# Optimization experiments

Measured on AMD Instinct MI355X. Metric: run time of the kernel, lower is better.

## Reference

```python
import jax, jax.numpy as jnp
import numpy as np

LEAKY_SLOPE = 0.01  # torch nn.LeakyReLU default


def leaky_relu(x):
    return jnp.where(x >= 0, x, LEAKY_SLOPE * x)


def rgcn_conv(x, edge_index, edge_type, w_rel, w_root, b_conv):
    # PyG RGCNConv: out = x @ W_root + b + sum_r mean_{edges of rel r into i}(x_src @ W_r)
    n = x.shape[0]
    src, dst = edge_index[0], edge_index[1]
    out = x @ w_root + b_conv
    num_rel = w_rel.shape[0]
    for r in range(num_rel):  # small fixed relation count
        mask = (edge_type == r)
        msg = x[src] @ w_rel[r]                      # [E, H]
        msg = jnp.where(mask[:, None], msg, 0.0)
        agg = jax.ops.segment_sum(msg, dst, num_segments=n)          # [N, H]
        cnt = jax.ops.segment_sum(mask.astype(x.dtype), dst, num_segments=n)
        out = out + agg / jnp.maximum(cnt, 1.0)[:, None]             # mean aggr
    return out


def setup_inputs() -> dict:
    key = jax.random.key(0)
    ks = jax.random.split(key, 10)
    N, E, D_IN, H, OUT, R = 50000, 600000, 768, 128, 3, 2
    s_in = 1.0 / np.sqrt(D_IN)
    s_h = 1.0 / np.sqrt(H)
    return {
        "feature": jax.random.normal(ks[0], (N, D_IN), dtype=jnp.float32),
        "edge_index": jax.random.randint(ks[1], (2, E), 0, N, dtype=jnp.int64),
        "edge_type": jax.random.randint(ks[2], (E,), 0, R, dtype=jnp.int64),
        "w_in": jax.random.uniform(ks[3], (D_IN, H), jnp.float32, -s_in, s_in),
        "b_in": jax.random.uniform(ks[4], (H,), jnp.float32, -s_in, s_in),
        "w_rel": jax.random.uniform(ks[5], (R, H, H), jnp.float32, -s_h, s_h),
        "w_root": jax.random.uniform(ks[6], (H, H), jnp.float32, -s_h, s_h),
        "b_conv": jnp.zeros((H,), jnp.float32),
        "w_out": jax.random.uniform(ks[7], (H, OUT), jnp.float32, -s_h, s_h),
        "b_out": jax.random.uniform(ks[8], (OUT,), jnp.float32, -s_h, s_h),
    }


def reference(feature, edge_index, edge_type, w_in, b_in, w_rel, w_root, b_conv, w_out, b_out):
    x = leaky_relu(feature @ w_in + b_in)
    # NOTE: original forward applies rgcn1 twice (shared weights); dropout is
    # identity at inference; rgcn2/linear_relu_output1 are unused.
    x = rgcn_conv(x, edge_index, edge_type, w_rel, w_root, b_conv)
    x = rgcn_conv(x, edge_index, edge_type, w_rel, w_root, b_conv)
    return x @ w_out + b_out
```

## Files before the change

kernel.cpp:

```cpp
#include <hip/hip_runtime.h>

#define H 128
#define CAP 64

typedef _Float16 f16x8 __attribute__((ext_vector_type(8)));
typedef float    f32x4 __attribute__((ext_vector_type(4)));

__global__ __launch_bounds__(256) void hist_fill(const int* __restrict__ src,
    const int* __restrict__ dst, const int* __restrict__ et,
    int* __restrict__ cnt, int* __restrict__ elist, int E, int N)
{
    int e = blockIdx.x * 256 + threadIdx.x;
    if (e >= E) return;
    int s = src[e], d = dst[e], t = et[e];
    int b = t * N + d;
    int pos = atomicAdd(&cnt[b], 1);
    if (pos < CAP) elist[(size_t)b * CAP + pos] = s;
}

__global__ __launch_bounds__(256) void prep_w(const float* __restrict__ w_in,
    const float* __restrict__ w_root, const float* __restrict__ w_rel,
    _Float16* __restrict__ wInT, _Float16* __restrict__ w3T, int K)
{
    int idx = blockIdx.x * 256 + threadIdx.x;
    int tot1 = K * H;
    if (idx < tot1) {
        int k = idx >> 7, c = idx & 127;
        int o = ((k >> 3) << 10) + (c << 3) + (k & 7);
        wInT[o] = (_Float16)w_in[idx];
    } else {
        int i2 = idx - tot1;
        if (i2 < 3 * H * H) {
            int m = i2 / (H * H), r2 = i2 - m * (H * H);
            int c = r2 >> 7, k = r2 & 127;
            const float* s = (m == 0) ? w_root : (w_rel + (size_t)(m - 1) * H * H);
            w3T[i2] = (_Float16)s[(size_t)k * H + c];
        }
    }
}

__device__ __forceinline__ f16x8 cvt8(float4 v0, float4 v1) {
    f16x8 t;
    t[0] = (_Float16)v0.x; t[1] = (_Float16)v0.y; t[2] = (_Float16)v0.z; t[3] = (_Float16)v0.w;
    t[4] = (_Float16)v1.x; t[5] = (_Float16)v1.y; t[6] = (_Float16)v1.z; t[7] = (_Float16)v1.w;
    return t;
}

__global__ __launch_bounds__(256, 3) void gemm_big(const float* __restrict__ A,
    const _Float16* __restrict__ WP, const float* __restrict__ bias,
    _Float16* __restrict__ C16, int M, int K)
{
    const int tid = threadIdx.x;
    const int w   = tid >> 6;
    const int l   = tid & 63;
    const int l15 = l & 15;
    const int q   = l >> 4;
    const int wrow = blockIdx.x * 64 + w * 16;

    int r0 = wrow + l15; if (r0 >= M) r0 = M - 1;
    const float* ap = A + (size_t)r0 * K + q * 8;
    const _Float16* bp = WP + ((size_t)q * H + l15) * 8;

    float bj[8];
#pragma unroll
    for (int j = 0; j < 8; j++) bj[j] = bias[j * 16 + l15];

    f32x4 acc[8];
    const f32x4 z4 = {0.f, 0.f, 0.f, 0.f};
#pragma unroll
    for (int j = 0; j < 8; j++) acc[j] = z4;

    float4 aA0, aA1; f16x8 bA[8];
    float4 aB0, aB1; f16x8 bB[8];

    aA0 = *(const float4*)(ap);
    aA1 = *(const float4*)(ap + 4);
#pragma unroll
    for (int j = 0; j < 8; j++) bA[j] = *(const f16x8*)(bp + j * 128);

    const int steps = K / 32;
    for (int s = 0; s < steps; s += 2) {
        {
            const int k1 = (s + 1) * 32;
            aB0 = *(const float4*)(ap + k1);
            aB1 = *(const float4*)(ap + k1 + 4);
            const _Float16* nb = bp + (size_t)(s + 1) * 4096;
#pragma unroll
            for (int j = 0; j < 8; j++) bB[j] = *(const f16x8*)(nb + j * 128);
        }
        {
            f16x8 af = cvt8(aA0, aA1);
#pragma unroll
            for (int j = 0; j < 8; j++)
                acc[j] = __builtin_amdgcn_mfma_f32_16x16x32_f16(af, bA[j], acc[j], 0, 0, 0);
        }
        if (s + 2 < steps) {
            const int k2 = (s + 2) * 32;
            aA0 = *(const float4*)(ap + k2);
            aA1 = *(const float4*)(ap + k2 + 4);
            const _Float16* nb = bp + (size_t)(s + 2) * 4096;
#pragma unroll
            for (int j = 0; j < 8; j++) bA[j] = *(const f16x8*)(nb + j * 128);
        }
        {
            f16x8 af = cvt8(aB0, aB1);
#pragma unroll
            for (int j = 0; j < 8; j++)
                acc[j] = __builtin_amdgcn_mfma_f32_16x16x32_f16(af, bB[j], acc[j], 0, 0, 0);
        }
    }

#pragma unroll
    for (int rg = 0; rg < 4; rg++) {
        int row = wrow + q * 4 + rg;
        if (row < M) {
#pragma unroll
            for (int j = 0; j < 8; j++) {
                float v = acc[j][rg] + bj[j];
                v = (v >= 0.f) ? v : 0.01f * v;
                C16[(size_t)row * H + j * 16 + l15] = (_Float16)v;
            }
        }
    }
}

__global__ __launch_bounds__(512) void gemm3(const _Float16* __restrict__ X16,
    const _Float16* __restrict__ W3, const float* __restrict__ bias,
    float* __restrict__ Y, _Float16* __restrict__ Hh, int M, int mtiles,
    size_t NH)
{
    const int w   = threadIdx.x >> 6;
    const int l   = threadIdx.x & 63;
    const int l15 = l & 15;
    const int q   = l >> 4;
    const int col = w * 16 + l15;

    f16x8 bf[3][4];
#pragma unroll
    for (int m = 0; m < 3; m++) {
        const _Float16* wpp = W3 + (size_t)m * H * H + (size_t)col * H + q * 8;
#pragma unroll
        for (int c = 0; c < 4; c++) bf[m][c] = *(const f16x8*)(wpp + c * 32);
    }
    const float bj = bias[col];

    int t = blockIdx.x;
    if (t >= mtiles) return;
    f16x8 xf[4];
    {
        const _Float16* xp = X16 + ((size_t)t * 16 + l15) * H + q * 8;
#pragma unroll
        for (int c = 0; c < 4; c++) xf[c] = *(const f16x8*)(xp + c * 32);
    }

    const f32x4 z4 = {0.f, 0.f, 0.f, 0.f};
    while (true) {
        int tn = t + gridDim.x;
        bool more = tn < mtiles;
        f16x8 xnf[4];
        if (more) {
            const _Float16* xp = X16 + ((size_t)tn * 16 + l15) * H + q * 8;
#pragma unroll
            for (int c = 0; c < 4; c++) xnf[c] = *(const f16x8*)(xp + c * 32);
        }

        f32x4 a0 = z4, a1 = z4, a2 = z4;
#pragma unroll
        for (int c = 0; c < 4; c++) {
            a0 = __builtin_amdgcn_mfma_f32_16x16x32_f16(xf[c], bf[0][c], a0, 0, 0, 0);
            a1 = __builtin_amdgcn_mfma_f32_16x16x32_f16(xf[c], bf[1][c], a1, 0, 0, 0);
            a2 = __builtin_amdgcn_mfma_f32_16x16x32_f16(xf[c], bf[2][c], a2, 0, 0, 0);
        }

#pragma unroll
        for (int rg = 0; rg < 4; rg++) {
            int row = t * 16 + q * 4 + rg;
            if (row < M) {
                Y [(size_t)row * H + col]      = a0[rg] + bj;
                Hh[(size_t)row * H + col]      = (_Float16)a1[rg];
                Hh[NH + (size_t)row * H + col] = (_Float16)a2[rg];
            }
        }
        if (!more) break;
        t = tn;
#pragma unroll
        for (int c = 0; c < 4; c++) xf[c] = xnf[c];
    }
}

template<int DO_OUT>
__global__ __launch_bounds__(256) void gather_mean(const float* __restrict__ Y,
    const _Float16* __restrict__ h, const int* __restrict__ elist,
    const int* __restrict__ cnt, _Float16* __restrict__ xn, int N, size_t NH,
    const float* __restrict__ Wo, const float* __restrict__ bo,
    float* __restrict__ out)
{
    int wv = blockIdx.x * 4 + (threadIdx.x >> 6);
    int l  = threadIdx.x & 63;
    if (wv >= N) return;

    int d0r = cnt[wv], d1r = cnt[N + wv];
    int d0 = d0r < CAP ? d0r : CAP;
    int d1 = d1r < CAP ? d1r : CAP;
    float inv0 = d0r > 0 ? 1.f / (float)d0r : 0.f;
    float inv1 = d1r > 0 ? 1.f / (float)d1r : 0.f;
    const int* l0 = elist + (size_t)wv * CAP;
    const int* l1 = elist + ((size_t)N + wv) * CAP;
    const int tot = d0 + d1;

    const int eo = l >> 4;
    const int c8 = (l & 15) * 8;

    float wo0[8], wo1[8], wo2[8];
    if (DO_OUT) {
#pragma unroll
        for (int j = 0; j < 8; j++) {
            wo0[j] = Wo[(c8 + j) * 3 + 0];
            wo1[j] = Wo[(c8 + j) * 3 + 1];
            wo2[j] = Wo[(c8 + j) * 3 + 2];
        }
    }

    float acc[8];
#pragma unroll
    for (int j = 0; j < 8; j++) acc[j] = 0.f;

    const f16x8 zv = {};
    for (int p = eo; p < tot; p += 16) {
        int p1 = p + 4, p2 = p + 8, p3 = p + 12;
        bool fA = p < d0;
        int   sA  = fA ? l0[p] : l1[p - d0];
        float scA = fA ? inv0 : inv1;
        f16x8 vA  = *(const f16x8*)&h[(fA ? (size_t)0 : NH) + (size_t)sA * H + c8];
        f16x8 vB = zv, vC = zv, vD = zv;
        float scB = 0.f, scC = 0.f, scD = 0.f;
        if (p1 < tot) {
            bool f = p1 < d0;
            int s = f ? l0[p1] : l1[p1 - d0];
            scB = f ? inv0 : inv1;
            vB = *(const f16x8*)&h[(f ? (size_t)0 : NH) + (size_t)s * H + c8];
        }
        if (p2 < tot) {
            bool f = p2 < d0;
            int s = f ? l0[p2] : l1[p2 - d0];
            scC = f ? inv0 : inv1;
            vC = *(const f16x8*)&h[(f ? (size_t)0 : NH) + (size_t)s * H + c8];
        }
        if (p3 < tot) {
            bool f = p3 < d0;
            int s = f ? l0[p3] : l1[p3 - d0];
            scD = f ? inv0 : inv1;
            vD = *(const f16x8*)&h[(f ? (size_t)0 : NH) + (size_t)s * H + c8];
        }
#pragma unroll
        for (int j = 0; j < 8; j++)
            acc[j] += scA * (float)vA[j] + scB * (float)vB[j]
                    + scC * (float)vC[j] + scD * (float)vD[j];
    }

#pragma unroll
    for (int j = 0; j < 8; j++) {
        acc[j] += __shfl_xor(acc[j], 16);
        acc[j] += __shfl_xor(acc[j], 32);
    }

    float4 y0 = *(const float4*)&Y[(size_t)wv * H + c8];
    float4 y1 = *(const float4*)&Y[(size_t)wv * H + c8 + 4];
    float xv[8];
    xv[0] = acc[0] + y0.x; xv[1] = acc[1] + y0.y;
    xv[2] = acc[2] + y0.z; xv[3] = acc[3] + y0.w;
    xv[4] = acc[4] + y1.x; xv[5] = acc[5] + y1.y;
    xv[6] = acc[6] + y1.z; xv[7] = acc[7] + y1.w;

    if (DO_OUT) {
        float p0 = 0.f, p1 = 0.f, p2 = 0.f;
#pragma unroll
        for (int j = 0; j < 8; j++) {
            p0 += xv[j] * wo0[j];
            p1 += xv[j] * wo1[j];
            p2 += xv[j] * wo2[j];
        }
#pragma unroll
        for (int off = 1; off <= 8; off <<= 1) {
            p0 += __shfl_xor(p0, off);
            p1 += __shfl_xor(p1, off);
            p2 += __shfl_xor(p2, off);
        }
        if (l == 0) {
            out[(size_t)wv * 3 + 0] = p0 + bo[0];
            out[(size_t)wv * 3 + 1] = p1 + bo[1];
            out[(size_t)wv * 3 + 2] = p2 + bo[2];
        }
    } else {
        if (eo == 0) {
            f16x8 o;
#pragma unroll
            for (int j = 0; j < 8; j++) o[j] = (_Float16)xv[j];
            *(f16x8*)&xn[(size_t)wv * H + c8] = o;
        }
    }
}

__global__ __launch_bounds__(256) void out_gemm(const _Float16* __restrict__ X16,
    const float* __restrict__ Wo, const float* __restrict__ bo,
    float* __restrict__ out, int N, int OUT)
{
    int row = blockIdx.x * 4 + (threadIdx.x >> 6);
    int lane = threadIdx.x & 63;
    if (row >= N) return;
    float a0 = (float)X16[(size_t)row * H + lane];
    float a1 = (float)X16[(size_t)row * H + 64 + lane];
    for (int c = 0; c < OUT; c++) {
        float p = a0 * Wo[lane * OUT + c] + a1 * Wo[(64 + lane) * OUT + c];
        for (int off = 32; off > 0; off >>= 1) p += __shfl_down(p, off);
        if (lane == 0) out[(size_t)row * OUT + c] = p + bo[c];
    }
}

extern "C" void kernel_launch(void* const* d_in, const int* in_sizes, int n_in,
                              void* d_out, int out_size, void* d_ws, size_t ws_size,
                              hipStream_t stream) {
    const float* feature = (const float*)d_in[0];
    const int*   ei      = (const int*)d_in[1];
    const int*   et      = (const int*)d_in[2];
    const float* w_in    = (const float*)d_in[3];
    const float* b_in    = (const float*)d_in[4];
    const float* w_rel   = (const float*)d_in[5];
    const float* w_root  = (const float*)d_in[6];
    const float* b_conv  = (const float*)d_in[7];
    const float* w_out   = (const float*)d_in[8];
    const float* b_out   = (const float*)d_in[9];

    const int HH   = in_sizes[4];
    const int D_IN = in_sizes[3] / HH;
    const int N    = in_sizes[0] / D_IN;
    const int E    = in_sizes[1] / 2;
    const int R    = in_sizes[5] / (HH * HH);
    const int OUT  = in_sizes[9];

    const size_t NH = (size_t)N * H;

    char* base = (char*)d_ws;
    _Float16* wInT = (_Float16*)base;
    _Float16* w3T  = wInT + (size_t)D_IN * HH;
    _Float16* x0   = w3T + (size_t)3 * HH * HH;
    _Float16* x1   = x0 + NH;
    _Float16* h    = x1 + NH;
    float* y       = (float*)(h + (size_t)R * NH);
    int* cnt       = (int*)(y + NH);
    int* elist     = cnt + (size_t)R * N;

    hipMemsetAsync(cnt, 0, sizeof(int) * (size_t)R * N, stream);
    prep_w<<<(D_IN * HH + 3 * HH * HH + 255) / 256, 256, 0, stream>>>(
        w_in, w_root, w_rel, wInT, w3T, D_IN);
    hist_fill<<<(E + 255) / 256, 256, 0, stream>>>(ei, ei + E, et, cnt, elist, E, N);

    gemm_big<<<(N + 63) / 64, 256, 0, stream>>>(feature, wInT, b_in, x0, N, D_IN);

    const int mtiles = (N + 15) / 16;
    const int gblocks = (N + 3) / 4;

    gemm3<<<1024, 512, 0, stream>>>(x0, w3T, b_conv, y, h, N, mtiles, NH);
    gather_mean<0><<<gblocks, 256, 0, stream>>>(y, h, elist, cnt, x1, N, NH,
                                                nullptr, nullptr, nullptr);
    gemm3<<<1024, 512, 0, stream>>>(x1, w3T, b_conv, y, h, N, mtiles, NH);
    if (OUT == 3) {
        gather_mean<1><<<gblocks, 256, 0, stream>>>(y, h, elist, cnt, x0, N, NH,
                                                    w_out, b_out, (float*)d_out);
    } else {
        gather_mean<0><<<gblocks, 256, 0, stream>>>(y, h, elist, cnt, x0, N, NH,
                                                    nullptr, nullptr, nullptr);
        out_gemm<<<gblocks, 256, 0, stream>>>(x0, w_out, b_out, (float*)d_out, N, OUT);
    }
}
```

Before: 463.3 us.

## Stage A tiles through double-buffered swizzled LDS in input GEMM

The input GEMM (N x 768 fp32 times 768 x 128) now loads A in 128-wide K chunks with coalesced float4 row reads, converts them to fp16 and stores them into a double-buffered, XOR-swizzled shared-memory tile. MFMA A fragments are then read from LDS. The next chunk's global loads overlap the current chunk's MFMAs. The aim is to replace the earlier strided per-lane 32-byte A reads with coalesced transfers. The cost is 32KB of LDS per block, which may limit occupancy under launch_bounds(256,3), plus a barrier per chunk. The B loads are also no longer prefetched one step ahead.

```diff
diff --git a/kernel.cpp b/kernel.cpp
--- a/kernel.cpp
+++ b/kernel.cpp
@@ -4,6 +4,7 @@
 #define CAP 64
 
 typedef _Float16 f16x8 __attribute__((ext_vector_type(8)));
+typedef _Float16 f16x4 __attribute__((ext_vector_type(4)));
 typedef float    f32x4 __attribute__((ext_vector_type(4)));
 
 __global__ __launch_bounds__(256) void hist_fill(const int* __restrict__ src,
@@ -39,26 +40,25 @@
     }
 }
 
-__device__ __forceinline__ f16x8 cvt8(float4 v0, float4 v1) {
-    f16x8 t;
-    t[0] = (_Float16)v0.x; t[1] = (_Float16)v0.y; t[2] = (_Float16)v0.z; t[3] = (_Float16)v0.w;
-    t[4] = (_Float16)v1.x; t[5] = (_Float16)v1.y; t[6] = (_Float16)v1.z; t[7] = (_Float16)v1.w;
-    return t;
-}
-
 __global__ __launch_bounds__(256, 3) void gemm_big(const float* __restrict__ A,
     const _Float16* __restrict__ WP, const float* __restrict__ bias,
     _Float16* __restrict__ C16, int M, int K)
 {
+    __shared__ _Float16 As[2][8192];
+
     const int tid = threadIdx.x;
     const int w   = tid >> 6;
     const int l   = tid & 63;
     const int l15 = l & 15;
     const int q   = l >> 4;
-    const int wrow = blockIdx.x * 64 + w * 16;
-
-    int r0 = wrow + l15; if (r0 >= M) r0 = M - 1;
-    const float* ap = A + (size_t)r0 * K + q * 8;
+    const int brow = blockIdx.x * 64;
+    const int wr   = w * 16;
+
+    const int srow = wr + (l >> 5);
+    const int sk4  = (l & 31) * 4;
+    const int slot = (l & 31) >> 1;
+    const int half = l & 1;
+
     const _Float16* bp = WP + ((size_t)q * H + l15) * 8;
 
     float bj[8];
@@ -70,49 +70,69 @@
 #pragma unroll
     for (int j = 0; j < 8; j++) acc[j] = z4;
 
-    float4 aA0, aA1; f16x8 bA[8];
-    float4 aB0, aB1; f16x8 bB[8];
-
-    aA0 = *(const float4*)(ap);
-    aA1 = *(const float4*)(ap + 4);
-#pragma unroll
-    for (int j = 0; j < 8; j++) bA[j] = *(const f16x8*)(bp + j * 128);
-
-    const int steps = K / 32;
-    for (int s = 0; s < steps; s += 2) {
+    const int chunks = K / 128;
+    float4 st[8];
+
+    {
+        const float* apc = A + sk4;
+#pragma unroll
+        for (int i = 0; i < 8; i++) {
+            int gr = brow + srow + i * 2; if (gr >= M) gr = M - 1;
+            st[i] = *(const float4*)(apc + (size_t)gr * K);
+        }
+#pragma unroll
+        for (int i = 0; i < 8; i++) {
+            int row = srow + i * 2;
+            int idx = slot * 512 + ((row ^ (slot & 7)) << 3) + half * 4;
+            f16x4 v; v[0] = (_Float16)st[i].x; v[1] = (_Float16)st[i].y;
+                     v[2] = (_Float16)st[i].z; v[3] = (_Float16)st[i].w;
+            *(f16x4*)&As[0][idx] = v;
+        }
+    }
+    __syncthreads();
+
+    for (int c = 0; c < chunks; c++) {
+        const bool more = (c + 1) < chunks;
+        if (more) {
+            const float* apc = A + (c + 1) * 128 + sk4;
+#pragma unroll
+            for (int i = 0; i < 8; i++) {
+                int gr = brow + srow + i * 2; if (gr >= M) gr = M - 1;
+                st[i] = *(const float4*)(apc + (size_t)gr * K);
+            }
+        }
         {
-            const int k1 = (s + 1) * 32;
-            aB0 = *(const float4*)(ap + k1);
-            aB1 = *(const float4*)(ap + k1 + 4);
-            const _Float16* nb = bp + (size_t)(s + 1) * 4096;
-#pragma unroll
-            for (int j = 0; j < 8; j++) bB[j] = *(const f16x8*)(nb + j * 128);
-        }
-        {
-            f16x8 af = cvt8(aA0, aA1);
-#pragma unroll
-            for (int j = 0; j < 8; j++)
-                acc[j] = __builtin_amdgcn_mfma_f32_16x16x32_f16(af, bA[j], acc[j], 0, 0, 0);
-        }
-        if (s + 2 < steps) {
-            const int k2 = (s + 2) * 32;
-            aA0 = *(const float4*)(ap + k2);
-            aA1 = *(const float4*)(ap + k2 + 4);
-            const _Float16* nb = bp + (size_t)(s + 2) * 4096;
-#pragma unroll
-            for (int j = 0; j < 8; j++) bA[j] = *(const f16x8*)(nb + j * 128);
-        }
-        {
-            f16x8 af = cvt8(aB0, aB1);
-#pragma unroll
-            for (int j = 0; j < 8; j++)
-                acc[j] = __builtin_amdgcn_mfma_f32_16x16x32_f16(af, bB[j], acc[j], 0, 0, 0);
-        }
+            const _Float16* __restrict__ buf = As[c & 1];
+#pragma unroll
+            for (int ks = 0; ks < 4; ks++) {
+                const int sl = ks * 4 + q;
+                f16x8 af = *(const f16x8*)&buf[sl * 512 + (((wr + l15) ^ (sl & 7)) << 3)];
+                const _Float16* bks = bp + (size_t)(c * 4 + ks) * 4096;
+                f16x8 bf[8];
+#pragma unroll
+                for (int j = 0; j < 8; j++) bf[j] = *(const f16x8*)(bks + j * 128);
+#pragma unroll
+                for (int j = 0; j < 8; j++)
+                    acc[j] = __builtin_amdgcn_mfma_f32_16x16x32_f16(af, bf[j], acc[j], 0, 0, 0);
+            }
+        }
+        if (more) {
+            _Float16* __restrict__ buf = As[(c + 1) & 1];
+#pragma unroll
+            for (int i = 0; i < 8; i++) {
+                int row = srow + i * 2;
+                int idx = slot * 512 + ((row ^ (slot & 7)) << 3) + half * 4;
+                f16x4 v; v[0] = (_Float16)st[i].x; v[1] = (_Float16)st[i].y;
+                         v[2] = (_Float16)st[i].z; v[3] = (_Float16)st[i].w;
+                *(f16x4*)&buf[idx] = v;
+            }
+        }
+        __syncthreads();
     }
 
 #pragma unroll
     for (int rg = 0; rg < 4; rg++) {
-        int row = wrow + q * 4 + rg;
+        int row = brow + wr + q * 4 + rg;
         if (row < M) {
 #pragma unroll
             for (int j = 0; j < 8; j++) {
```

New measurement: 452.1 us. 1.02x faster.
